# Performance work log

Hardware: AMD Instinct MI355X
Metric: run time of the kernel (lower is better)

## Reference

```python
import jax, jax.numpy as jnp
import numpy as np

D_MODEL = 1024
N_HEADS = 16
D_HEAD = D_MODEL // N_HEADS
B, T = 4, 2048


def layernorm(x, g, b, eps=1e-5):
    mu = jnp.mean(x, axis=-1, keepdims=True)
    var = jnp.mean((x - mu) ** 2, axis=-1, keepdims=True)
    return (x - mu) * jax.lax.rsqrt(var + eps) * g + b


def setup_inputs() -> dict:
    key = jax.random.key(0)
    ks = jax.random.split(key, 12)
    s_in = 1.0 / np.sqrt(D_MODEL)
    s_ff = 1.0 / np.sqrt(4 * D_MODEL)
    return {
        "x": jax.random.normal(ks[0], (B, T, D_MODEL), jnp.float32),
        "Wq": jax.random.normal(ks[1], (N_HEADS, D_MODEL, D_HEAD), jnp.float32) * s_in,
        "Wk": jax.random.normal(ks[2], (N_HEADS, D_MODEL, D_HEAD), jnp.float32) * s_in,
        "Wv": jax.random.normal(ks[3], (N_HEADS, D_MODEL, D_HEAD), jnp.float32) * s_in,
        "Wproj": jax.random.normal(ks[4], (D_MODEL, D_MODEL), jnp.float32) * s_in,
        "bproj": jnp.zeros((D_MODEL,), jnp.float32),
        "W1": jax.random.normal(ks[5], (D_MODEL, 4 * D_MODEL), jnp.float32) * s_in,
        "b1": jnp.zeros((4 * D_MODEL,), jnp.float32),
        "W2": jax.random.normal(ks[6], (4 * D_MODEL, D_MODEL), jnp.float32) * s_ff,
        "b2": jnp.zeros((D_MODEL,), jnp.float32),
        "g1": jnp.ones((D_MODEL,), jnp.float32),
        "beta1": jnp.zeros((D_MODEL,), jnp.float32),
        "g2": jnp.ones((D_MODEL,), jnp.float32),
        "beta2": jnp.zeros((D_MODEL,), jnp.float32),
    }


def reference(x, Wq, Wk, Wv, Wproj, bproj, W1, b1, W2, b2, g1, beta1, g2, beta2):
    Bb, Tt, C = x.shape
    # x = ln1(x); residual uses the NORMALIZED x (quirk of original module)
    x1 = layernorm(x, g1, beta1)
    # all heads at once: [B,H,T,Dh]
    q = jnp.einsum("btd,hdk->bhtk", x1, Wq)
    k = jnp.einsum("btd,hdk->bhtk", x1, Wk)
    v = jnp.einsum("btd,hdk->bhtk", x1, Wv)
    # NOTE: original scales by 1/sqrt(C) with C = d_model, not d_head
    wei = jnp.einsum("bhtk,bhsk->bhts", q, k) / np.sqrt(C).astype(np.float32)
    causal = jnp.tril(jnp.ones((Tt, Tt), bool))
    wei = jnp.where(causal, wei, -jnp.inf)
    wei = jax.nn.softmax(wei, axis=-1)
    attn = jnp.einsum("bhts,bhsk->bhtk", wei, v)  # [B,H,T,Dh]
    attn = attn.transpose(0, 2, 1, 3).reshape(Bb, Tt, C)  # concat heads
    sa = attn @ Wproj + bproj
    x2 = x1 + sa
    # x = ln2(x); residual again uses the normalized tensor
    x3 = layernorm(x2, g2, beta2)
    h = jax.nn.relu(x3 @ W1 + b1)
    ff = h @ W2 + b2
    return x3 + ff
```

## Files before the change

kernel.cpp:

```cpp
#include <hip/hip_runtime.h>
#include <cstdint>

typedef _Float16 f16;
typedef __attribute__((ext_vector_type(8))) _Float16 f16x8;
typedef __attribute__((ext_vector_type(4))) _Float16 f16x4;
typedef __attribute__((ext_vector_type(2))) _Float16 f16x2;
typedef __attribute__((ext_vector_type(4))) float f32x4;
typedef __attribute__((ext_vector_type(16))) float f32x16;

#define D_MODEL 1024
#define T_SEQ   2048
#define NTOK    8192
#define DFF     4096
#define DHEAD   64

struct alignas(16) H8 { f16 h[8]; };

__device__ __forceinline__ void load_lds16(const void* gp, void* lp) {
  __builtin_amdgcn_global_load_lds(
      (const __attribute__((address_space(1))) unsigned int*)(unsigned long long)(uintptr_t)gp,
      (__attribute__((address_space(3))) unsigned int*)(unsigned int)(uintptr_t)lp,
      16, 0, 0);
}

__device__ __forceinline__ void phase_bar() {
  asm volatile("" ::: "memory");
  __builtin_amdgcn_sched_barrier(0);
  __builtin_amdgcn_s_barrier();
  __builtin_amdgcn_sched_barrier(0);
  asm volatile("" ::: "memory");
}

__device__ __forceinline__ void wait_vm2() {
  asm volatile("s_waitcnt vmcnt(2)" ::: "memory");
  __builtin_amdgcn_sched_barrier(0);
}
__device__ __forceinline__ void wait_vm0() {
  asm volatile("s_waitcnt vmcnt(0)" ::: "memory");
  __builtin_amdgcn_sched_barrier(0);
}

__global__ __launch_bounds__(256) void transpose_all(
    const float* __restrict__ Wq, const float* __restrict__ Wk,
    const float* __restrict__ Wv, const float* __restrict__ Wproj,
    const float* __restrict__ W1, const float* __restrict__ W2,
    f16* __restrict__ Wqkv_t, f16* __restrict__ Wproj_t,
    f16* __restrict__ W1_t, f16* __restrict__ W2_t)
{
  __shared__ float tile[32][33];
  int b = blockIdx.x;
  const float* in; f16* out; int rows, cols, r0, c0;
  if (b < 3072) {
    int j = b >> 10;
    int local = b & 1023;
    int slice = local >> 6;
    int tl = local & 63;
    in  = (j == 0 ? Wq : (j == 1 ? Wk : Wv)) + (size_t)slice * 65536;
    out = Wqkv_t + (size_t)j * 1024 * 1024 + (size_t)slice * 65536;
    rows = 1024; cols = 64;
    r0 = (tl & 31) * 32; c0 = (tl >> 5) * 32;
  } else if (b < 4096) {
    int tl = b - 3072;
    in = Wproj; out = Wproj_t; rows = 1024; cols = 1024;
    r0 = (tl & 31) * 32; c0 = (tl >> 5) * 32;
  } else if (b < 8192) {
    int tl = b - 4096;
    in = W1; out = W1_t; rows = 1024; cols = 4096;
    r0 = (tl & 31) * 32; c0 = (tl >> 5) * 32;
  } else {
    int tl = b - 8192;
    in = W2; out = W2_t; rows = 4096; cols = 1024;
    r0 = (tl & 127) * 32; c0 = (tl >> 7) * 32;
  }
  int tx = threadIdx.x & 31, ty = threadIdx.x >> 5;
  #pragma unroll
  for (int i = 0; i < 4; ++i)
    tile[ty + i*8][tx] = in[(size_t)(r0 + ty + i*8)*cols + c0 + tx];
  __syncthreads();
  #pragma unroll
  for (int i = 0; i < 4; ++i)
    out[(size_t)(c0 + ty + i*8)*rows + r0 + tx] = (f16)tile[tx][ty + i*8];
}

__global__ __launch_bounds__(256) void ln_kernel(
    const float* __restrict__ x, const float* __restrict__ g, const float* __restrict__ b,
    float* __restrict__ outf, f16* __restrict__ outh)
{
  int row = blockIdx.x;
  const float* xr = x + (size_t)row * D_MODEL;
  int tid = threadIdx.x;
  float v[4];
  float s = 0.f;
  #pragma unroll
  for (int i = 0; i < 4; ++i) { v[i] = xr[tid + i*256]; s += v[i]; }
  #pragma unroll
  for (int off = 32; off > 0; off >>= 1) s += __shfl_down(s, off, 64);
  __shared__ float red1[4], red2[4];
  if ((tid & 63) == 0) red1[tid >> 6] = s;
  __syncthreads();
  float mean = (red1[0] + red1[1] + red1[2] + red1[3]) * (1.f / D_MODEL);
  float s2 = 0.f;
  #pragma unroll
  for (int i = 0; i < 4; ++i) { float d = v[i] - mean; s2 += d * d; }
  #pragma unroll
  for (int off = 32; off > 0; off >>= 1) s2 += __shfl_down(s2, off, 64);
  if ((tid & 63) == 0) red2[tid >> 6] = s2;
  __syncthreads();
  float var = (red2[0] + red2[1] + red2[2] + red2[3]) * (1.f / D_MODEL);
  float rstd = rsqrtf(var + 1e-5f);
  #pragma unroll
  for (int i = 0; i < 4; ++i) {
    int c = tid + i*256;
    float y = (v[i] - mean) * rstd * g[c] + b[c];
    outf[(size_t)row*D_MODEL + c] = y;
    outh[(size_t)row*D_MODEL + c] = (f16)y;
  }
}


#define STAGE_H(gbase, h, ldst, k0)                                            \
  { _Pragma("unroll")                                                          \
    for (int j_ = 0; j_ < 2; ++j_) {                                           \
      int c_  = tid + j_*512;                                                  \
      int rr_ = c_ >> 3;                                                       \
      int cg_ = (c_ & 7) ^ (rr_ & 7);                                          \
      load_lds16((gbase) + (size_t)((h)*128 + rr_) * K + (k0) + cg_*8,         \
                 (ldst) + (h)*128*64 + (size_t)(c_ & ~63) * 8);                \
    } }

#define LDS_A(bsel, mp)                                                        \
  { _Pragma("unroll")                                                          \
    for (int i_ = 0; i_ < 2; ++i_)                                             \
      _Pragma("unroll")                                                        \
      for (int ks_ = 0; ks_ < 4; ++ks_)                                        \
        fa[i_][ks_] = *(const f16x8*)(&As[bsel][                               \
            (wm + ((mp)*2 + i_)*32 + rl)*64 + (((ks_*2 + hl) ^ sw)*8)]); }

#define LDS_B(bsel, ni, fb)                                                    \
  { _Pragma("unroll")                                                          \
    for (int ks_ = 0; ks_ < 4; ++ks_)                                          \
      fb[ks_] = *(const f16x8*)(&Bs[bsel][                                     \
          (wn + (ni)*32 + rl)*64 + (((ks_*2 + hl) ^ sw)*8)]); }

#define MFMA8(mp, ni, fb)                                                      \
  { __builtin_amdgcn_s_setprio(1);                                             \
    _Pragma("unroll")                                                          \
    for (int ks_ = 0; ks_ < 4; ++ks_) {                                        \
      acc[(mp)*2+0][ni] = __builtin_amdgcn_mfma_f32_32x32x16_f16(              \
          fa[0][ks_], fb[ks_], acc[(mp)*2+0][ni], 0, 0, 0);                    \
      acc[(mp)*2+1][ni] = __builtin_amdgcn_mfma_f32_32x32x16_f16(              \
          fa[1][ks_], fb[ks_], acc[(mp)*2+1][ni], 0, 0, 0);                    \
    }                                                                          \
    __builtin_amdgcn_s_setprio(0); }

template<int MODE, int BN>
__global__ __launch_bounds__(512, 2) void gemm8(
    const f16* __restrict__ A, const f16* __restrict__ BT, int K,
    const float* __restrict__ bias, const float* __restrict__ resid,
    float* __restrict__ outf, f16* __restrict__ o0, f16* __restrict__ o1, f16* __restrict__ o2)
{
  constexpr int BM  = 256;
  constexpr int NWN = BN / 64;
  constexpr int MI  = (BM / (8 / NWN)) / 32;

  __shared__ __align__(16) f16 As[2][BM * 64];
  __shared__ __align__(16) f16 Bs[2][BN * 64];

  int tid  = threadIdx.x;
  int lane = tid & 63;
  int wave = tid >> 6;
  int rl = lane & 31, hl = lane >> 5;
  int sw = rl & 7;
  int wmi = wave / NWN, wni = wave % NWN;
  int wm = wmi * (MI * 32), wn = wni * 64;

  int gx  = gridDim.x;
  int gy  = gridDim.y;
  int nwg = gx * gy;
  int lin = blockIdx.x + gx * blockIdx.y;
  int sid = (nwg & 7) == 0 ? ((lin & 7) * (nwg >> 3) + (lin >> 3)) : lin;
  int bx  = sid / gy, by = sid % gy;

  size_t row0 = (size_t)bx * BM, col0 = (size_t)by * BN;
  const f16* a_base = A  + row0 * K;
  const f16* b_base = BT + col0 * K;
  int NT = K >> 6;

  f32x16 acc[MI][2];
  #pragma unroll
  for (int i = 0; i < MI; ++i)
    #pragma unroll
    for (int j = 0; j < 2; ++j)
      acc[i][j] = (f32x16)(0.f);

  f16x8 fa[2][4], fb0[4], fb1[4];

  if constexpr (BN == 256) {
    STAGE_H(a_base, 0, &As[0][0], 0);
    STAGE_H(a_base, 1, &As[0][0], 0);
    STAGE_H(b_base, 0, &Bs[0][0], 0);
    STAGE_H(b_base, 1, &Bs[0][0], 0);
    if (NT > 1) { STAGE_H(a_base, 0, &As[1][0], 64); wait_vm2(); }
    else        { wait_vm0(); }
    phase_bar();

    for (int t = 0; t < NT; ++t) {
      int cur = t & 1, nxt = cur ^ 1;
      int k1 = (t + 1) << 6, k2 = (t + 2) << 6;
      bool s1 = (t + 1) < NT, s2 = (t + 2) < NT;
      LDS_A(cur, 0); LDS_B(cur, 0, fb0);
      if (s1) STAGE_H(a_base, 1, &As[nxt][0], k1);
      phase_bar();
      MFMA8(0, 0, fb0);
      phase_bar();
      LDS_B(cur, 1, fb1);
      if (s1) STAGE_H(b_base, 0, &Bs[nxt][0], k1);
      phase_bar();
      MFMA8(0, 1, fb1);
      phase_bar();
      LDS_A(cur, 1);
      if (s1) STAGE_H(b_base, 1, &Bs[nxt][0], k1);
      phase_bar();
      MFMA8(1, 0, fb0);
      phase_bar();
      if (s2) STAGE_H(a_base, 0, &As[cur][0], k2);
      phase_bar();
      MFMA8(1, 1, fb1);
      if (s2) wait_vm2(); else wait_vm0();
      phase_bar();
    }
  } else {
    STAGE_H(a_base, 0, &As[0][0], 0);
    STAGE_H(a_base, 1, &As[0][0], 0);
    STAGE_H(b_base, 0, &Bs[0][0], 0);
    if (NT > 1) { STAGE_H(a_base, 0, &As[1][0], 64); wait_vm2(); }
    else        { wait_vm0(); }
    phase_bar();

    for (int t = 0; t < NT; t += 2) {
      int k1 = (t + 1) << 6, k2 = (t + 2) << 6, k3 = (t + 3) << 6;
      bool s1 = (t + 1) < NT, s2 = (t + 2) < NT, s3 = (t + 3) < NT;
      LDS_A(0, 0); LDS_B(0, 0, fb0);
      if (s1) { STAGE_H(a_base, 1, &As[1][0], k1); STAGE_H(b_base, 0, &Bs[1][0], k1); }
      phase_bar();
      MFMA8(0, 0, fb0);
      phase_bar();
      LDS_B(0, 1, fb1);
      if (s2) STAGE_H(a_base, 0, &As[0][0], k2);
      phase_bar();
      MFMA8(0, 1, fb1);
      if (s2) wait_vm2(); else wait_vm0();
      phase_bar();
      if (!s1) break;
      LDS_A(1, 0); LDS_B(1, 0, fb0);
      if (s2) { STAGE_H(a_base, 1, &As[0][0], k2); STAGE_H(b_base, 0, &Bs[0][0], k2); }
      phase_bar();
      MFMA8(0, 0, fb0);
      phase_bar();
      LDS_B(1, 1, fb1);
      if (s3) STAGE_H(a_base, 0, &As[1][0], k3);
      phase_bar();
      MFMA8(0, 1, fb1);
      if (s3) wait_vm2(); else wait_vm0();
      phase_bar();
    }
  }

  int rb = hl * 4;
  #pragma unroll
  for (int mi = 0; mi < MI; ++mi) {
    #pragma unroll
    for (int ni = 0; ni < 2; ++ni) {
      #pragma unroll
      for (int r = 0; r < 16; ++r) {
        size_t grow = row0 + wm + mi*32 + rb + (r & 3) + 8 * (r >> 2);
        size_t gcol = col0 + wn + ni*32 + rl;
        float v = acc[mi][ni][r];
        if constexpr (MODE == 0) {
          int sel = (int)(gcol >> 10);
          int hh  = ((int)gcol >> 6) & 15;
          int dd  = (int)gcol & 63;
          f16* dst = (sel == 0) ? o0 : ((sel == 1) ? o1 : o2);
          if (sel == 0) v *= 0.045084229f;
          size_t bh = (grow >> 11) * 16 + hh;
          dst[(bh * T_SEQ + (grow & 2047)) * DHEAD + dd] = (f16)v;
        } else if constexpr (MODE == 1 || MODE == 3) {
          size_t idx = grow * D_MODEL + gcol;
          outf[idx] = v + bias[gcol] + resid[idx];
        } else {
          float t = v + bias[gcol];
          o0[grow * (size_t)DFF + gcol] = (f16)(t > 0.f ? t : 0.f);
        }
      }
    }
  }
}

__global__ __launch_bounds__(256) void attn_mfma(
    const f16* __restrict__ qb, const f16* __restrict__ kb,
    const f16* __restrict__ vb, f16* __restrict__ attnb)
{
  constexpr int KT  = 64;
  constexpr int LDK = 72;
  __shared__ __align__(16) f16 Kl[2][KT * LDK];
  __shared__ __align__(16) f16 Vt[2][DHEAD * LDK];
  __shared__ __align__(16) f16 Pt[4 * 32 * LDK];

  int tid  = threadIdx.x;
  int lane = tid & 63, wave = tid >> 6;
  int n    = lane & 15, quad = lane >> 4;
  int quad4 = quad * 4;
  int bh   = blockIdx.y;

  const f16* qg = qb + (size_t)bh * T_SEQ * DHEAD;
  const f16* kg = kb + (size_t)bh * T_SEQ * DHEAD;
  const f16* vg = vb + (size_t)bh * T_SEQ * DHEAD;
  f16* Ptw = Pt + wave * 32 * LDK;
  size_t orow = (size_t)(bh >> 4) * T_SEQ;
  int hcol = (bh & 15) * DHEAD;

  int skey0 = tid >> 3,  sdq = tid & 7;
  int kp = tid & 31, dblk = tid >> 5;

  #pragma unroll
  for (int pass = 0; pass < 2; ++pass) {
    int qi = pass == 0 ? (15 - (int)blockIdx.x) : (int)blockIdx.x;
    int qw = qi * 128 + wave * 32;

    f16x8 qfrag[2][2];
    #pragma unroll
    for (int ni = 0; ni < 2; ++ni)
      #pragma unroll
      for (int kj = 0; kj < 2; ++kj)
        qfrag[ni][kj] = *(const f16x8*)(qg + (size_t)(qw + ni*16 + n)*DHEAD + kj*32 + quad*8);

    f32x4 o[2][4];
    #pragma unroll
    for (int mb = 0; mb < 2; ++mb)
      #pragma unroll
      for (int di = 0; di < 4; ++di) o[mb][di] = f32x4{0.f,0.f,0.f,0.f};
    float lsum[2] = {0.f, 0.f};

    int ntiles = 2 * qi + 2;

    uint4 kpre0 = *(const uint4*)(kg + (size_t)skey0 * DHEAD + sdq * 8);
    uint4 kpre1 = *(const uint4*)(kg + (size_t)(skey0 + 32) * DHEAD + sdq * 8);
    H8 vpa = *(const H8*)(vg + (size_t)(2*kp) * DHEAD + dblk * 8);
    H8 vpb = *(const H8*)(vg + (size_t)(2*kp) * DHEAD + DHEAD + dblk * 8);
    *(uint4*)(&Kl[0][0] + skey0 * LDK + sdq * 8) = kpre0;
    *(uint4*)(&Kl[0][0] + (skey0 + 32) * LDK + sdq * 8) = kpre1;
    #pragma unroll
    for (int e = 0; e < 8; ++e) {
      f16x2 pk2; pk2[0] = vpa.h[e]; pk2[1] = vpb.h[e];
      *(f16x2*)(&Vt[0][0] + (dblk*8 + e) * LDK + 2*kp) = pk2;
    }
    if (ntiles > 1) {
      kpre0 = *(const uint4*)(kg + (size_t)(KT + skey0) * DHEAD + sdq * 8);
      kpre1 = *(const uint4*)(kg + (size_t)(KT + skey0 + 32) * DHEAD + sdq * 8);
      vpa = *(const H8*)(vg + (size_t)(KT + 2*kp) * DHEAD + dblk * 8);
      vpb = *(const H8*)(vg + (size_t)(KT + 2*kp) * DHEAD + DHEAD + dblk * 8);
    }
    __syncthreads();

    for (int kt = 0; kt < ntiles; ++kt) {
      int kt0 = kt * KT;
      if (kt + 1 < ntiles) {
        f16* Kn = &Kl[(kt + 1) & 1][0];
        f16* Vn = &Vt[(kt + 1) & 1][0];
        *(uint4*)(Kn + skey0 * LDK + sdq * 8) = kpre0;
        *(uint4*)(Kn + (skey0 + 32) * LDK + sdq * 8) = kpre1;
        #pragma unroll
        for (int e = 0; e < 8; ++e) {
          f16x2 pk2; pk2[0] = vpa.h[e]; pk2[1] = vpb.h[e];
          *(f16x2*)(Vn + (dblk*8 + e) * LDK + 2*kp) = pk2;
        }
        if (kt + 2 < ntiles) {
          int nt0 = kt0 + 2 * KT;
          kpre0 = *(const uint4*)(kg + (size_t)(nt0 + skey0) * DHEAD + sdq * 8);
          kpre1 = *(const uint4*)(kg + (size_t)(nt0 + skey0 + 32) * DHEAD + sdq * 8);
          vpa = *(const H8*)(vg + (size_t)(nt0 + 2*kp) * DHEAD + dblk * 8);
          vpb = *(const H8*)(vg + (size_t)(nt0 + 2*kp) * DHEAD + DHEAD + dblk * 8);
        }
      }

      if (kt0 <= qw + 31) {
        const f16* Kc = &Kl[kt & 1][0];
        const f16* Vc = &Vt[kt & 1][0];
        bool need_mask = (kt0 + KT - 1) > qw;

        f32x4 st[4][2];
        #pragma unroll
        for (int mi = 0; mi < 4; ++mi)
          #pragma unroll
          for (int ni = 0; ni < 2; ++ni) st[mi][ni] = f32x4{0.f,0.f,0.f,0.f};
        __builtin_amdgcn_s_setprio(1);
        #pragma unroll
        for (int kj = 0; kj < 2; ++kj) {
          #pragma unroll
          for (int mi = 0; mi < 4; ++mi) {
            f16x8 kf = *(const f16x8*)(Kc + (mi*16 + n) * LDK + kj*32 + quad*8);
            #pragma unroll
            for (int ni = 0; ni < 2; ++ni)
              st[mi][ni] = __builtin_amdgcn_mfma_f32_16x16x32_f16(kf, qfrag[ni][kj], st[mi][ni], 0, 0, 0);
          }
        }
        __builtin_amdgcn_s_setprio(0);

        #pragma unroll
        for (int ni = 0; ni < 2; ++ni) {
          #pragma unroll
          for (int mi = 0; mi < 4; ++mi) {
            f16x4 pk;
            #pragma unroll
            for (int r = 0; r < 4; ++r) {
              float sv = st[mi][ni][r];
              if (need_mask) {
                int key = kt0 + mi*16 + quad4 + r;
                int qq  = qw  + ni*16 + n;
                if (key > qq) sv = -1e30f;
              }
              float p = __builtin_amdgcn_exp2f(sv);
              lsum[ni] += p;
              pk[r] = (f16)p;
            }
            *(f16x4*)(Ptw + (ni*16 + n) * LDK + mi*16 + quad4) = pk;
          }
        }

        __builtin_amdgcn_s_setprio(1);
        #pragma unroll
        for (int kj = 0; kj < 2; ++kj) {
          f16x8 pf[2];
          #pragma unroll
          for (int mb = 0; mb < 2; ++mb)
            pf[mb] = *(const f16x8*)(Ptw + (mb*16 + n) * LDK + kj*32 + quad*8);
          #pragma unroll
          for (int di = 0; di < 4; ++di) {
            f16x8 vf = *(const f16x8*)(Vc + (di*16 + n) * LDK + kj*32 + quad*8);
            #pragma unroll
            for (int mb = 0; mb < 2; ++mb)
              o[mb][di] = __builtin_amdgcn_mfma_f32_16x16x32_f16(pf[mb], vf, o[mb][di], 0, 0, 0);
          }
        }
        __builtin_amdgcn_s_setprio(0);
      }
      __syncthreads();
    }

    #pragma unroll
    for (int ni = 0; ni < 2; ++ni) {
      lsum[ni] += __shfl_xor(lsum[ni], 16, 64);
      lsum[ni] += __shfl_xor(lsum[ni], 32, 64);
    }
    #pragma unroll
    for (int mb = 0; mb < 2; ++mb) {
      #pragma unroll
      for (int r = 0; r < 4; ++r) {
        float lv  = __shfl(lsum[mb], quad4 + r, 64);
        float inv = 1.f / lv;
        int t = qw + mb*16 + quad4 + r;
        #pragma unroll
        for (int di = 0; di < 4; ++di)
          attnb[(orow + t) * D_MODEL + hcol + di*16 + n] = (f16)(o[mb][di][r] * inv);
      }
    }
  }
}

extern "C" void kernel_launch(void* const* d_in, const int* in_sizes, int n_in,
                              void* d_out, int out_size, void* d_ws, size_t ws_size,
                              hipStream_t stream)
{
  const float* x     = (const float*)d_in[0];
  const float* Wq    = (const float*)d_in[1];
  const float* Wk    = (const float*)d_in[2];
  const float* Wv    = (const float*)d_in[3];
  const float* Wproj = (const float*)d_in[4];
  const float* bproj = (const float*)d_in[5];
  const float* W1    = (const float*)d_in[6];
  const float* b1    = (const float*)d_in[7];
  const float* W2    = (const float*)d_in[8];
  const float* b2    = (const float*)d_in[9];
  const float* g1    = (const float*)d_in[10];
  const float* bt1   = (const float*)d_in[11];
  const float* g2    = (const float*)d_in[12];
  const float* bt2   = (const float*)d_in[13];
  float* out = (float*)d_out;
  (void)in_sizes; (void)n_in; (void)out_size; (void)ws_size;

  char* ws = (char*)d_ws;
  const size_t SZ_H16 = (size_t)NTOK * D_MODEL * 2;
  const size_t SZ_F32 = (size_t)NTOK * D_MODEL * 4;
  f16*   qb      = (f16*)(ws + 0);
  f16*   kb      = (f16*)(ws + 1 * SZ_H16);
  f16*   vb      = (f16*)(ws + 2 * SZ_H16);
  f16*   attnb   = (f16*)(ws + 3 * SZ_H16);
  f16*   hbuf    = (f16*)(ws + 0);
  float* x1f     = (float*)(ws + 4 * SZ_H16);
  f16*   x1h     = (f16*)(ws + 4 * SZ_H16 + SZ_F32);
  float* x3f     = (float*)(ws + 5 * SZ_H16 + SZ_F32);
  f16*   x3h     = (f16*)(ws + 5 * SZ_H16 + 2 * SZ_F32);
  char*  wb      = ws + 6 * SZ_H16 + 2 * SZ_F32;
  f16*   Wqkv_t  = (f16*)(wb);
  f16*   Wproj_t = (f16*)(wb + (size_t)3072*1024*2);
  f16*   W1_t    = (f16*)(wb + (size_t)(3072+1024)*1024*2);
  f16*   W2_t    = (f16*)(wb + (size_t)(3072+1024+4096)*1024*2);

  dim3 blk(256), blk5(512);
  transpose_all<<<dim3(12288), blk, 0, stream>>>(Wq, Wk, Wv, Wproj, W1, W2,
                                                 Wqkv_t, Wproj_t, W1_t, W2_t);
  ln_kernel<<<NTOK, blk, 0, stream>>>(x, g1, bt1, x1f, x1h);
  gemm8<0,128><<<dim3(32, 24), blk5, 0, stream>>>(x1h, Wqkv_t, 1024, nullptr, nullptr, nullptr, qb, kb, vb);
  attn_mfma<<<dim3(8, 64), blk, 0, stream>>>(qb, kb, vb, attnb);
  gemm8<1,128><<<dim3(32, 8), blk5, 0, stream>>>(attnb, Wproj_t, 1024, bproj, x1f, x1f, nullptr, nullptr, nullptr);
  ln_kernel<<<NTOK, blk, 0, stream>>>(x1f, g2, bt2, x3f, x3h);
  gemm8<2,256><<<dim3(32, 16), blk5, 0, stream>>>(x3h, W1_t, 1024, b1, nullptr, nullptr, hbuf, nullptr, nullptr);
  gemm8<3,128><<<dim3(32, 8), blk5, 0, stream>>>(hbuf, W2_t, 4096, b2, x3f, out, nullptr, nullptr, nullptr);
}
```

Baseline: 495.6 us.

## Compute softmax row sums via ones-row MFMA and swap attention grid order

Appends a ones row to the transposed V tile in shared memory so an extra MFMA accumulates the softmax denominator, replacing per-element scalar adds and the final cross-lane reductions. The f16 conversion of probabilities now uses packed round-toward-zero conversion. The attention grid is transposed so consecutive blocks belong to different batch-heads, which changes workgroup scheduling and cache locality. This adds some shared memory and extra MFMAs per tile, and the row sum is now taken from f16-rounded probabilities rather than fp32 ones.

Result: faster. 472.0 us (-4.8%).

```diff
diff --git a/kernel.cpp b/kernel.cpp
--- a/kernel.cpp
+++ b/kernel.cpp
@@ -303,14 +303,15 @@
   constexpr int KT  = 64;
   constexpr int LDK = 72;
   __shared__ __align__(16) f16 Kl[2][KT * LDK];
-  __shared__ __align__(16) f16 Vt[2][DHEAD * LDK];
+  __shared__ __align__(16) f16 Vt[2][(DHEAD+16) * LDK];
   __shared__ __align__(16) f16 Pt[4 * 32 * LDK];
 
   int tid  = threadIdx.x;
   int lane = tid & 63, wave = tid >> 6;
   int n    = lane & 15, quad = lane >> 4;
   int quad4 = quad * 4;
-  int bh   = blockIdx.y;
+  int bh   = blockIdx.x;
+  int bxq  = blockIdx.y;
 
   const f16* qg = qb + (size_t)bh * T_SEQ * DHEAD;
   const f16* kg = kb + (size_t)bh * T_SEQ * DHEAD;
@@ -322,9 +323,18 @@
   int skey0 = tid >> 3,  sdq = tid & 7;
   int kp = tid & 31, dblk = tid >> 5;
 
+  {
+    int row = 64 + (tid >> 4);
+    int colg = (tid & 15) * 4;
+    f16 oneval = (f16)((tid >> 4) == 0 ? 1.0f : 0.0f);
+    f16x4 fill = {oneval, oneval, oneval, oneval};
+    *(f16x4*)(&Vt[0][0] + row * LDK + colg) = fill;
+    *(f16x4*)(&Vt[1][0] + row * LDK + colg) = fill;
+  }
+
   #pragma unroll
   for (int pass = 0; pass < 2; ++pass) {
-    int qi = pass == 0 ? (15 - (int)blockIdx.x) : (int)blockIdx.x;
+    int qi = pass == 0 ? (15 - bxq) : bxq;
     int qw = qi * 128 + wave * 32;
 
     f16x8 qfrag[2][2];
@@ -335,11 +345,13 @@
         qfrag[ni][kj] = *(const f16x8*)(qg + (size_t)(qw + ni*16 + n)*DHEAD + kj*32 + quad*8);
 
     f32x4 o[2][4];
+    f32x4 o4[2];
     #pragma unroll
-    for (int mb = 0; mb < 2; ++mb)
+    for (int mb = 0; mb < 2; ++mb) {
       #pragma unroll
       for (int di = 0; di < 4; ++di) o[mb][di] = f32x4{0.f,0.f,0.f,0.f};
-    float lsum[2] = {0.f, 0.f};
+      o4[mb] = f32x4{0.f,0.f,0.f,0.f};
+    }
 
     int ntiles = 2 * qi + 2;
 
@@ -410,7 +422,7 @@
         for (int ni = 0; ni < 2; ++ni) {
           #pragma unroll
           for (int mi = 0; mi < 4; ++mi) {
-            f16x4 pk;
+            float pv[4];
             #pragma unroll
             for (int r = 0; r < 4; ++r) {
               float sv = st[mi][ni][r];
@@ -419,10 +431,11 @@
                 int qq  = qw  + ni*16 + n;
                 if (key > qq) sv = -1e30f;
               }
-              float p = __builtin_amdgcn_exp2f(sv);
-              lsum[ni] += p;
-              pk[r] = (f16)p;
+              pv[r] = __builtin_amdgcn_exp2f(sv);
             }
+            f16x2 lo = __builtin_bit_cast(f16x2, __builtin_amdgcn_cvt_pkrtz(pv[0], pv[1]));
+            f16x2 hi = __builtin_bit_cast(f16x2, __builtin_amdgcn_cvt_pkrtz(pv[2], pv[3]));
+            f16x4 pk; pk[0] = lo[0]; pk[1] = lo[1]; pk[2] = hi[0]; pk[3] = hi[1];
             *(f16x4*)(Ptw + (ni*16 + n) * LDK + mi*16 + quad4) = pk;
           }
         }
@@ -441,6 +454,10 @@
             for (int mb = 0; mb < 2; ++mb)
               o[mb][di] = __builtin_amdgcn_mfma_f32_16x16x32_f16(pf[mb], vf, o[mb][di], 0, 0, 0);
           }
+          f16x8 vfo = *(const f16x8*)(Vc + (64 + n) * LDK + kj*32 + quad*8);
+          #pragma unroll
+          for (int mb = 0; mb < 2; ++mb)
+            o4[mb] = __builtin_amdgcn_mfma_f32_16x16x32_f16(pf[mb], vfo, o4[mb], 0, 0, 0);
         }
         __builtin_amdgcn_s_setprio(0);
       }
@@ -448,15 +465,10 @@
     }
 
     #pragma unroll
-    for (int ni = 0; ni < 2; ++ni) {
-      lsum[ni] += __shfl_xor(lsum[ni], 16, 64);
-      lsum[ni] += __shfl_xor(lsum[ni], 32, 64);
-    }
-    #pragma unroll
     for (int mb = 0; mb < 2; ++mb) {
       #pragma unroll
       for (int r = 0; r < 4; ++r) {
-        float lv  = __shfl(lsum[mb], quad4 + r, 64);
+        float lv  = __shfl(o4[mb][r], quad * 16, 64);
         float inv = 1.f / lv;
         int t = qw + mb*16 + quad4 + r;
         #pragma unroll
@@ -511,7 +523,7 @@
                                                  Wqkv_t, Wproj_t, W1_t, W2_t);
   ln_kernel<<<NTOK, blk, 0, stream>>>(x, g1, bt1, x1f, x1h);
   gemm8<0,128><<<dim3(32, 24), blk5, 0, stream>>>(x1h, Wqkv_t, 1024, nullptr, nullptr, nullptr, qb, kb, vb);
-  attn_mfma<<<dim3(8, 64), blk, 0, stream>>>(qb, kb, vb, attnb);
+  attn_mfma<<<dim3(64, 8), blk, 0, stream>>>(qb, kb, vb, attnb);
   gemm8<1,128><<<dim3(32, 8), blk5, 0, stream>>>(attnb, Wproj_t, 1024, bproj, x1f, x1f, nullptr, nullptr, nullptr);
   ln_kernel<<<NTOK, blk, 0, stream>>>(x1f, g2, bt2, x3f, x3h);
   gemm8<2,256><<<dim3(32, 16), blk5, 0, stream>>>(x3h, W1_t, 1024, b1, nullptr, nullptr, hbuf, nullptr, nullptr);
```
